# Performance work log

Measured on AMD Instinct MI355X. Metric: run time of the kernel, lower is better.

## Reference

```python
import jax, jax.numpy as jnp
import numpy as np

EDGES = np.array([[0,13],[0,1],[0,4],[0,10],[0,7],[13,14],[14,15],[15,16],[1,2],[2,3],
                  [3,17],[4,5],[5,6],[6,18],[10,11],[11,12],[12,19],[7,8],[8,9],[9,20]])
N = 21
EPS = 1e-5


def _build_adj():
    # adj_mx_from_edges: symmetric binary adjacency + self-loops, row-normalized (D^-1 (A+I))
    A = np.zeros((N, N), np.float32)
    A[EDGES[:, 0], EDGES[:, 1]] = 1.0
    A = np.maximum(A, A.T)
    A = A + np.eye(N, dtype=np.float32)
    A = A / A.sum(1, keepdims=True)
    return A


def setup_inputs() -> dict:
    key = jax.random.key(0)
    ks = jax.random.split(key, 10)
    B, C, H, W = 64, 256, 64, 64
    s = 0.05
    return {
        "feature_s": jax.random.normal(ks[0], (B, C, H, W), jnp.float32),
        "target_s": jax.random.uniform(ks[1], (B, N, H, W), jnp.float32),
        "adj": jnp.asarray(_build_adj()),
        "bn_gamma": jnp.ones((N,), jnp.float32),
        "bn_beta": jnp.zeros((N,), jnp.float32),
        "gru_wx": s * jax.random.normal(ks[2], (256, 768), jnp.float32),
        "gru_wh": s * jax.random.normal(ks[3], (256, 768), jnp.float32),
        "gru_bx": jnp.zeros((768,), jnp.float32),
        "gru_bh": jnp.zeros((768,), jnp.float32),
        "w_g1": s * jax.random.normal(ks[4], (2, 256, 256), jnp.float32),
        "b_g1": jnp.zeros((256,), jnp.float32),
        "w_g2": s * jax.random.normal(ks[5], (2, 256, 256), jnp.float32),
        "b_g2": jnp.zeros((256,), jnp.float32),
        "w_out": s * jax.random.normal(ks[6], (2, 256, 3), jnp.float32),
        "b_out": jnp.zeros((3,), jnp.float32),
    }


def _batchnorm1d(x, gamma, beta):
    # x: [B, 21, C]; BatchNorm1d over channel dim 21 (stats over batch and length)
    mean = jnp.mean(x, axis=(0, 2), keepdims=True)
    var = jnp.var(x, axis=(0, 2), keepdims=True)
    xn = (x - mean) * jax.lax.rsqrt(var + EPS)
    return xn * gamma[None, :, None] + beta[None, :, None]


def _gru(x, wx, wh, bx, bh):
    # standard GRU scanned over the 21-joint axis; x: [B, N, 256] -> [B, N, 256]
    B, n, Hd = x.shape
    xg = jnp.einsum('bnc,ch->bnh', x, wx) + bx  # [B, N, 3H]

    def step(h, xg_t):
        hg = h @ wh + bh
        r = jax.nn.sigmoid(xg_t[..., :Hd] + hg[..., :Hd])
        z = jax.nn.sigmoid(xg_t[..., Hd:2 * Hd] + hg[..., Hd:2 * Hd])
        ncand = jnp.tanh(xg_t[..., 2 * Hd:] + r * hg[..., 2 * Hd:])
        h_new = (1.0 - z) * ncand + z * h
        return h_new, h_new

    h0 = jnp.zeros((B, Hd), x.dtype)
    _, ys = jax.lax.scan(step, h0, jnp.swapaxes(xg, 0, 1))
    return jnp.swapaxes(ys, 0, 1)


def _laplacian(adj):
    # normalized Laplacian L = I - D^{-1/2} A D^{-1/2}
    d = adj.sum(-1)
    dinv = jnp.where(d > 0, jax.lax.rsqrt(jnp.where(d > 0, d, 1.0)), 0.0)
    return jnp.eye(N, dtype=adj.dtype) - dinv[:, None] * adj * dinv[None, :]


def _chebconv(x, L, w, b):
    # K=2 Chebyshev conv: T0 = I, T1 = L ->  x @ W0 + (L x) @ W1 + b
    return jnp.einsum('bnc,co->bno', x, w[0]) + jnp.einsum('nm,bmc,co->bno', L, x, w[1]) + b


def reference(feature_s, target_s, adj, bn_gamma, bn_beta,
              gru_wx, gru_wh, gru_bx, gru_bh,
              w_g1, b_g1, w_g2, b_g2, w_out, b_out):
    B, C, H, W = feature_s.shape
    # batched correlation: [B, 21, HW] x [B, HW, C] -> [B, 21, C]
    q = jnp.einsum('bjp,bcp->bjc',
                   target_s.reshape(B, N, H * W),
                   feature_s.reshape(B, C, H * W))
    q = _batchnorm1d(q, bn_gamma, bn_beta)
    q = jnp.where(q > 0, q, 0.1 * q)  # LeakyReLU(0.1)
    q = _gru(q, gru_wx, gru_wh, gru_bx, gru_bh)
    # _ResChebGC: two graph convs with ReLU + residual (dropout = identity in eval)
    L = _laplacian(adj)
    h = jax.nn.relu(_chebconv(q, L, w_g1, b_g1))
    h = jax.nn.relu(_chebconv(h, L, w_g2, b_g2))
    x = q + h
    return _chebconv(x, L, w_out, b_out)  # [B, 21, 3]
```

## Files before the change

### kernel.cpp

```cpp
#include <hip/hip_runtime.h>
#include <cstdint>

#define B   64
#define NJ  21
#define CHN 256
#define HW  4096
#define G3  768

typedef _Float16 f16x8 __attribute__((ext_vector_type(8)));
typedef float    f32x4 __attribute__((ext_vector_type(4)));
typedef _Float16 f16x2 __attribute__((ext_vector_type(2)));
typedef __fp16   fp16x2v __attribute__((ext_vector_type(2)));
union PKU { fp16x2v h; unsigned u; };
union HU { unsigned u; f16x2 h; };
union FRU { f16x8 v; unsigned u[4]; };

static __device__ inline unsigned pack_f16(float a, float b){
  HU u; u.h.x = (_Float16)a; u.h.y = (_Float16)b; return u.u;
}

static __device__ inline float fdot2f(unsigned wu, unsigned hu, float acc){
  HU w, h; w.u = wu; h.u = hu;
#if __has_builtin(__builtin_amdgcn_fdot2)
  return __builtin_amdgcn_fdot2(w.h, h.h, acc, false);
#else
  return acc + (float)w.h.x*(float)h.h.x + (float)w.h.y*(float)h.h.y;
#endif
}

__global__ __launch_bounds__(64) void k_lap(const float* __restrict__ adj, float* __restrict__ L){
  __shared__ float dinv[NJ];
  int t = threadIdx.x;
  if (t < NJ){
    float s = 0.f;
    for (int j=0;j<NJ;j++) s += adj[t*NJ+j];
    dinv[t] = s > 0.f ? 1.f/sqrtf(s) : 0.f;
  }
  __syncthreads();
  for (int idx=t; idx<NJ*NJ; idx+=64){
    int i = idx/NJ, j = idx%NJ;
    L[idx] = (i==j ? 1.f : 0.f) - dinv[i]*adj[idx]*dinv[j];
  }
}

__global__ __launch_bounds__(512,4) void k_corr6(const float* __restrict__ T,
    const float* __restrict__ F, _Float16* __restrict__ P){
  int bid = blockIdx.x;
  int nb = bid & 1, kb = (bid>>1)&3, b = bid>>3;
  int t = threadIdx.x;
  int w = t>>6, l = t&63;
  __shared__ __align__(16) unsigned short Tl[32*1024];

  for (int i=t; i<5632; i+=512){
    int r = 21 + (i>>9), pr = i & 511;
    int addr = (r*2048 + pr*4) ^ ((r&7)<<4);
    *(unsigned*)((char*)Tl + addr) = 0u;
  }
  {
    const float2* Tp = (const float2*)(T + (size_t)b*NJ*HW + (size_t)kb*1024);
    for (int i=t; i<21*512; i+=512){
      int r = i>>9, pr = i & 511;
      float2 v = Tp[(size_t)r*2048 + pr];
      PKU pk; pk.h = __builtin_amdgcn_cvt_pkrtz(v.x, v.y);
      int addr = (r*2048 + pr*4) ^ ((r&7)<<4);
      *(unsigned*)((char*)Tl + addr) = pk.u;
    }
  }
  __syncthreads();

  int cl = l & 15, kg = l >> 4;
  const float4* Fp = (const float4*)(F + ((size_t)b*CHN + nb*128 + w*16 + cl)*HW
                                       + (size_t)kb*1024) + kg*2;
  f32x4 acc0 = {0.f,0.f,0.f,0.f}, acc1 = {0.f,0.f,0.f,0.f};
  int r = l & 15;
  int swz = (r&7)<<4;

  #pragma unroll 4
  for (int chunk=0; chunk<32; ++chunk){
    float4 f0 = Fp[chunk*8];
    float4 f1 = Fp[chunk*8 + 1];
    FRU bf;
    bf.u[0] = pack_f16(f0.x, f0.y);
    bf.u[1] = pack_f16(f0.z, f0.w);
    bf.u[2] = pack_f16(f1.x, f1.y);
    bf.u[3] = pack_f16(f1.z, f1.w);
    int kbyte = chunk*64 + kg*16;
    f16x8 a0 = *(const f16x8*)((const char*)Tl + ((r*2048      + kbyte) ^ swz));
    f16x8 a1 = *(const f16x8*)((const char*)Tl + (((r+16)*2048 + kbyte) ^ swz));
    acc0 = __builtin_amdgcn_mfma_f32_16x16x32_f16(a0, bf.v, acc0, 0, 0, 0);
    acc1 = __builtin_amdgcn_mfma_f32_16x16x32_f16(a1, bf.v, acc1, 0, 0, 0);
  }

  int cbase = nb*128 + w*16 + (l&15);
  #pragma unroll
  for (int i=0;i<4;i++){
    int row0 = (l>>4)*4 + i;
    if (row0 < 21)
      P[(((size_t)kb*64 + b)*21 + row0)*256 + cbase] = (_Float16)acc0[i];
    int row1 = row0 + 16;
    if (row1 < 21)
      P[(((size_t)kb*64 + b)*21 + row1)*256 + cbase] = (_Float16)acc1[i];
  }
}

__global__ __launch_bounds__(256) void k_stats(const _Float16* __restrict__ P,
    float* __restrict__ q, float* __restrict__ stats){
  int j = blockIdx.x, t = threadIdx.x;
  const size_t KSTRIDE = (size_t)64*21*256;
  float s = 0.f, ss = 0.f;
  for (int b=0;b<B;b++){
    size_t i0 = ((size_t)b*21 + j)*256 + t;
    float v = (float)P[i0] + (float)P[KSTRIDE + i0]
            + (float)P[2*KSTRIDE + i0] + (float)P[3*KSTRIDE + i0];
    q[((size_t)b*NJ + j)*CHN + t] = v;
    s += v; ss += v*v;
  }
  #pragma unroll
  for (int o=32;o>0;o>>=1){ s += __shfl_down(s,o); ss += __shfl_down(ss,o); }
  __shared__ float sb[4], ssb[4];
  int wid = t>>6;
  if ((t&63)==0){ sb[wid]=s; ssb[wid]=ss; }
  __syncthreads();
  if (t==0){
    float S  = sb[0]+sb[1]+sb[2]+sb[3];
    float SS = ssb[0]+ssb[1]+ssb[2]+ssb[3];
    float mean = S * (1.f/16384.f);
    float var  = SS * (1.f/16384.f) - mean*mean;
    stats[j]      = mean;
    stats[NJ + j] = 1.f/sqrtf(var + 1e-5f);
  }
}

__global__ __launch_bounds__(256) void k_xg(const float* __restrict__ q,
    const float* __restrict__ stats, const float* __restrict__ gamma, const float* __restrict__ beta,
    const float* __restrict__ wx, const float* __restrict__ bx, float* __restrict__ xg){
  int b = blockIdx.x/3, sl = blockIdx.x%3;
  int t = threadIdx.x;
  int col = sl*256 + t;
  __shared__ float xn[NJ][CHN];
  for (int idx=t; idx<NJ*CHN; idx+=256){
    int j = idx >> 8;
    float v = (q[(size_t)b*NJ*CHN + idx] - stats[j]) * stats[NJ+j];
    v = v * gamma[j] + beta[j];
    xn[j][idx & 255] = v > 0.f ? v : 0.1f*v;
  }
  __syncthreads();
  float acc[NJ];
  #pragma unroll
  for (int j=0;j<NJ;j++) acc[j]=0.f;
  for (int c=0;c<CHN;c++){
    float wv = wx[(size_t)c*G3 + col];
    #pragma unroll
    for (int j=0;j<NJ;j++) acc[j] += xn[j][c]*wv;
  }
  float bv = bx[col];
  #pragma unroll
  for (int j=0;j<NJ;j++) xg[((size_t)b*NJ+j)*G3 + col] = acc[j] + bv;
}

__global__ __launch_bounds__(256) void k_pack(const float* __restrict__ wh, unsigned* __restrict__ whp){
  int idx = blockIdx.x*256 + threadIdx.x;
  int c2 = idx / G3, col = idx % G3;
  float w0 = wh[(size_t)(2*c2)*G3 + col];
  float w1 = wh[(size_t)(2*c2+1)*G3 + col];
  whp[idx] = pack_f16(w0, w1);
}

__global__ __launch_bounds__(768,3) void k_gru(const unsigned* __restrict__ whp,
    const float* __restrict__ bh, const float* __restrict__ xg, float* __restrict__ gout){
  int b = blockIdx.x;
  int col = threadIdx.x;
  int l = col & 63;
  __shared__ float hf[256];
  __shared__ float lr[256], lz[256];
  unsigned wr[64];
  #pragma unroll
  for (int i=0;i<64;i++) wr[i] = whp[i*G3 + col];
  const unsigned* wsp = whp + 64*G3 + col;
  float bhv = bh[col];
  if (col < 256) hf[col] = 0.f;
  unsigned hv0 = 0u, hv1 = 0u;
  float xv_next = xg[((size_t)b*NJ + 0)*G3 + col];
  __syncthreads();
  for (int step=0; step<NJ; ++step){
    float xvc = xv_next;
    if (step < NJ-1) xv_next = xg[((size_t)b*NJ + step+1)*G3 + col];
    float a0 = 0.f, a1 = 0.f;
    #pragma unroll
    for (int i=0;i<64;i++)
      a1 = fdot2f(wsp[(size_t)i*G3], __builtin_amdgcn_readlane(hv1, i), a1);
    #pragma unroll
    for (int i=0;i<64;i++)
      a0 = fdot2f(wr[i], __builtin_amdgcn_readlane(hv0, i), a0);
    float a = a0 + a1 + bhv;
    if (col < 256)      lr[col]     = 1.f/(1.f+__expf(-(xvc + a)));
    else if (col < 512) lz[col-256] = 1.f/(1.f+__expf(-(xvc + a)));
    __syncthreads();
    if (col >= 512){
      int i = col - 512;
      float nv = tanhf(xvc + lr[i]*a);
      float z  = lz[i];
      float hnew = (1.f - z)*nv + z*hf[i];
      gout[((size_t)b*NJ + step)*CHN + i] = hnew;
      hf[i] = hnew;
    }
    __syncthreads();
    float2 p0 = *(const float2*)&hf[2*l];
    float2 p1 = *(const float2*)&hf[128 + 2*l];
    hv0 = pack_f16(p0.x, p0.y);
    hv1 = pack_f16(p1.x, p1.y);
  }
}

__global__ __launch_bounds__(256) void k_cheb(const float* __restrict__ xin,
    const float* __restrict__ Lm, const float* __restrict__ W,
    const float* __restrict__ bvec, float* __restrict__ out){
  int b = blockIdx.x >> 2, oq = blockIdx.x & 3;
  int t = threadIdx.x;
  int ol = t & 63, ck = t >> 6;
  __shared__ float xs[NJ][CHN];
  __shared__ float lx[NJ][CHN];
  __shared__ float part[4][64][NJ];
  for (int idx=t; idx<NJ*CHN; idx+=256) xs[idx>>8][idx&255] = xin[(size_t)b*NJ*CHN + idx];
  __syncthreads();
  for (int idx=t; idx<NJ*CHN; idx+=256){
    int j = idx>>8, c = idx&255;
    float sacc = 0.f;
    #pragma unroll
    for (int m=0;m<NJ;m++) sacc += Lm[j*NJ+m]*xs[m][c];
    lx[j][c] = sacc;
  }
  __syncthreads();
  int o = oq*64 + ol;
  float acc[NJ];
  #pragma unroll
  for (int j=0;j<NJ;j++) acc[j]=0.f;
  const float* W0 = W;
  const float* W1 = W + CHN*CHN;
  for (int cc=0; cc<64; ++cc){
    int c = ck*64 + cc;
    float w0 = W0[(size_t)c*CHN + o];
    float w1 = W1[(size_t)c*CHN + o];
    #pragma unroll
    for (int j=0;j<NJ;j++){ acc[j] += xs[j][c]*w0; acc[j] += lx[j][c]*w1; }
  }
  #pragma unroll
  for (int j=0;j<NJ;j++) part[ck][ol][j] = acc[j];
  __syncthreads();
  for (int idx=t; idx<64*NJ; idx+=256){
    int o2 = idx & 63, j = idx >> 6;
    float s2 = part[0][o2][j]+part[1][o2][j]+part[2][o2][j]+part[3][o2][j] + bvec[oq*64+o2];
    s2 = s2 > 0.f ? s2 : 0.f;
    out[(size_t)b*NJ*CHN + j*CHN + oq*64 + o2] = s2;
  }
}

__global__ __launch_bounds__(64) void k_out(const float* __restrict__ gq, const float* __restrict__ h2,
    const float* __restrict__ Lm, const float* __restrict__ W, const float* __restrict__ bvec,
    float* __restrict__ out){
  int b = blockIdx.x, t = threadIdx.x;
  __shared__ float xs[NJ][CHN];
  __shared__ float lx[NJ][CHN];
  for (int idx=t; idx<NJ*CHN; idx+=64)
    xs[idx>>8][idx&255] = gq[(size_t)b*NJ*CHN+idx] + h2[(size_t)b*NJ*CHN+idx];
  __syncthreads();
  for (int idx=t; idx<NJ*CHN; idx+=64){
    int j = idx>>8, c = idx&255;
    float s = 0.f;
    #pragma unroll
    for (int m=0;m<NJ;m++) s += Lm[j*NJ+m]*xs[m][c];
    lx[j][c] = s;
  }
  __syncthreads();
  if (t < 63){
    int j = t/3, o = t%3;
    float acc = bvec[o];
    const float* W0 = W;
    const float* W1 = W + CHN*3;
    for (int c=0;c<CHN;c++){
      acc += xs[j][c]*W0[c*3+o];
      acc += lx[j][c]*W1[c*3+o];
    }
    out[(size_t)b*63 + t] = acc;
  }
}

extern "C" void kernel_launch(void* const* d_in, const int* in_sizes, int n_in,
                              void* d_out, int out_size, void* d_ws, size_t ws_size,
                              hipStream_t stream){
  const float* feat  = (const float*)d_in[0];
  const float* targ  = (const float*)d_in[1];
  const float* adj   = (const float*)d_in[2];
  const float* gamma = (const float*)d_in[3];
  const float* beta  = (const float*)d_in[4];
  const float* wx    = (const float*)d_in[5];
  const float* wh    = (const float*)d_in[6];
  const float* bx    = (const float*)d_in[7];
  const float* bh    = (const float*)d_in[8];
  const float* wg1   = (const float*)d_in[9];
  const float* bg1   = (const float*)d_in[10];
  const float* wg2   = (const float*)d_in[11];
  const float* bg2   = (const float*)d_in[12];
  const float* wout  = (const float*)d_in[13];
  const float* bout  = (const float*)d_in[14];

  float* ws   = (float*)d_ws;
  float* q     = ws + 0;
  float* stats = ws + 400000;
  float* Lw    = ws + 400128;
  float* xgw   = ws + 500000;
  float* gout  = ws + 1600000;
  float* h1    = ws + 2000000;
  float* h2b   = ws + 2400000;
  unsigned* whp = (unsigned*)(ws + 2800000);
  _Float16* P  = (_Float16*)(ws + 3000000);

  k_lap  <<<1,    64, 0, stream>>>(adj, Lw);
  k_pack <<<384, 256, 0, stream>>>(wh, whp);
  k_corr6<<<512, 512, 0, stream>>>(targ, feat, P);
  k_stats<<<21,  256, 0, stream>>>(P, q, stats);
  k_xg   <<<192, 256, 0, stream>>>(q, stats, gamma, beta, wx, bx, xgw);
  k_gru  <<<64,  768, 0, stream>>>(whp, bh, xgw, gout);
  k_cheb <<<256, 256, 0, stream>>>(gout, Lw, wg1, bg1, h1);
  k_cheb <<<256, 256, 0, stream>>>(h1,   Lw, wg2, bg2, h2b);
  k_out  <<<64,   64, 0, stream>>>(gout, h2b, Lw, wout, bout, (float*)d_out);
}
```

Before: 262.3 us.

## Stream feature tiles via async global-to-LDS loads with triple buffering in correlation kernel

The correlation kernel now splits HW into 8 K-chunks instead of 4, doubling the grid to 1024 blocks and halving each block's T tile in LDS. Feature loads go directly to LDS through global_load_lds into a 3-slot ring buffer per wave, with explicit vmcnt waits so loads stay in flight while the MFMAs run. The stats kernel now sums 8 partial products instead of 4. This trades more LDS use and twice as much partial-sum traffic for better memory-level parallelism on the bandwidth-bound feature stream.

```diff
diff --git a/kernel.cpp b/kernel.cpp
--- a/kernel.cpp
+++ b/kernel.cpp
@@ -28,6 +28,17 @@
 #endif
 }
 
+static __device__ __forceinline__ void gload_lds16(const float* g, float* l){
+#if __has_builtin(__builtin_amdgcn_global_load_lds)
+  __builtin_amdgcn_global_load_lds((const __attribute__((address_space(1))) void*)g,
+                                   (__attribute__((address_space(3))) void*)l, 16, 0, 0);
+#else
+  int lane = threadIdx.x & 63;
+  f32x4 v = *(const f32x4*)g;
+  *(f32x4*)((char*)l + lane*16) = v;
+#endif
+}
+
 __global__ __launch_bounds__(64) void k_lap(const float* __restrict__ adj, float* __restrict__ L){
   __shared__ float dinv[NJ];
   int t = threadIdx.x;
@@ -43,52 +54,66 @@
   }
 }
 
-__global__ __launch_bounds__(512,4) void k_corr6(const float* __restrict__ T,
+__global__ __launch_bounds__(512,4) void k_corr7(const float* __restrict__ T,
     const float* __restrict__ F, _Float16* __restrict__ P){
   int bid = blockIdx.x;
-  int nb = bid & 1, kb = (bid>>1)&3, b = bid>>3;
+  int nb = bid & 1, kb = (bid>>1)&7, b = bid>>4;
   int t = threadIdx.x;
   int w = t>>6, l = t&63;
-  __shared__ __align__(16) unsigned short Tl[32*1024];
-
-  for (int i=t; i<5632; i+=512){
-    int r = 21 + (i>>9), pr = i & 511;
-    int addr = (r*2048 + pr*4) ^ ((r&7)<<4);
-    *(unsigned*)((char*)Tl + addr) = 0u;
+  __shared__ __align__(16) unsigned short Tl[32*512];
+  __shared__ __align__(16) float Fl[8][3][512];
+
+  for (int i=t; i<2816; i+=512){
+    int r = 21 + i/256, wo = i%256;
+    *(unsigned*)((char*)Tl + (r*1024 + ((wo*4) ^ ((r&7)<<4)))) = 0u;
   }
   {
-    const float2* Tp = (const float2*)(T + (size_t)b*NJ*HW + (size_t)kb*1024);
-    for (int i=t; i<21*512; i+=512){
-      int r = i>>9, pr = i & 511;
+    const float2* Tp = (const float2*)(T + (size_t)b*NJ*HW + (size_t)kb*512);
+    for (int i=t; i<21*256; i+=512){
+      int r = i>>8, pr = i&255;
       float2 v = Tp[(size_t)r*2048 + pr];
       PKU pk; pk.h = __builtin_amdgcn_cvt_pkrtz(v.x, v.y);
-      int addr = (r*2048 + pr*4) ^ ((r&7)<<4);
-      *(unsigned*)((char*)Tl + addr) = pk.u;
+      *(unsigned*)((char*)Tl + (r*1024 + ((pr*4) ^ ((r&7)<<4)))) = pk.u;
     }
   }
   __syncthreads();
 
   int cl = l & 15, kg = l >> 4;
-  const float4* Fp = (const float4*)(F + ((size_t)b*CHN + nb*128 + w*16 + cl)*HW
-                                       + (size_t)kb*1024) + kg*2;
+  const float* gsrc = F + ((size_t)b*CHN + nb*128 + w*16 + cl)*HW + (size_t)kb*512 + kg*8;
+  float* slotbase = &Fl[w][0][0];
+
   f32x4 acc0 = {0.f,0.f,0.f,0.f}, acc1 = {0.f,0.f,0.f,0.f};
-  int r = l & 15;
+  int r = cl;
   int swz = (r&7)<<4;
-
-  #pragma unroll 4
-  for (int chunk=0; chunk<32; ++chunk){
-    float4 f0 = Fp[chunk*8];
-    float4 f1 = Fp[chunk*8 + 1];
+  const char* TlB = (const char*)Tl;
+
+  gload_lds16(gsrc + 0*32,     slotbase);
+  gload_lds16(gsrc + 0*32 + 4, slotbase + 256);
+  gload_lds16(gsrc + 1*32,     slotbase + 512);
+  gload_lds16(gsrc + 1*32 + 4, slotbase + 512 + 256);
+
+  #pragma unroll
+  for (int c=0; c<16; ++c){
+    int cc = (c+2 < 16) ? (c+2) : 15;
+    float* lpn = slotbase + ((c+2)%3)*512;
+    gload_lds16(gsrc + cc*32,     lpn);
+    gload_lds16(gsrc + cc*32 + 4, lpn + 256);
+    asm volatile("s_waitcnt vmcnt(4)" ::: "memory");
+    __builtin_amdgcn_sched_barrier(0);
+    const char* sp = (const char*)(slotbase + (c%3)*512);
+    f32x4 v0 = *(const f32x4*)(sp + l*16);
+    f32x4 v1 = *(const f32x4*)(sp + 1024 + l*16);
     FRU bf;
-    bf.u[0] = pack_f16(f0.x, f0.y);
-    bf.u[1] = pack_f16(f0.z, f0.w);
-    bf.u[2] = pack_f16(f1.x, f1.y);
-    bf.u[3] = pack_f16(f1.z, f1.w);
-    int kbyte = chunk*64 + kg*16;
-    f16x8 a0 = *(const f16x8*)((const char*)Tl + ((r*2048      + kbyte) ^ swz));
-    f16x8 a1 = *(const f16x8*)((const char*)Tl + (((r+16)*2048 + kbyte) ^ swz));
+    bf.u[0] = pack_f16(v0[0], v0[1]);
+    bf.u[1] = pack_f16(v0[2], v0[3]);
+    bf.u[2] = pack_f16(v1[0], v1[1]);
+    bf.u[3] = pack_f16(v1[2], v1[3]);
+    int kbyte = c*64 + kg*16;
+    f16x8 a0 = *(const f16x8*)(TlB + (r*1024      + (kbyte ^ swz)));
+    f16x8 a1 = *(const f16x8*)(TlB + ((r+16)*1024 + (kbyte ^ swz)));
     acc0 = __builtin_amdgcn_mfma_f32_16x16x32_f16(a0, bf.v, acc0, 0, 0, 0);
     acc1 = __builtin_amdgcn_mfma_f32_16x16x32_f16(a1, bf.v, acc1, 0, 0, 0);
+    __builtin_amdgcn_sched_barrier(0);
   }
 
   int cbase = nb*128 + w*16 + (l&15);
@@ -110,8 +135,9 @@
   float s = 0.f, ss = 0.f;
   for (int b=0;b<B;b++){
     size_t i0 = ((size_t)b*21 + j)*256 + t;
-    float v = (float)P[i0] + (float)P[KSTRIDE + i0]
-            + (float)P[2*KSTRIDE + i0] + (float)P[3*KSTRIDE + i0];
+    float v = 0.f;
+    #pragma unroll
+    for (int k=0;k<8;k++) v += (float)P[k*KSTRIDE + i0];
     q[((size_t)b*NJ + j)*CHN + t] = v;
     s += v; ss += v*v;
   }
@@ -317,7 +343,7 @@
 
   k_lap  <<<1,    64, 0, stream>>>(adj, Lw);
   k_pack <<<384, 256, 0, stream>>>(wh, whp);
-  k_corr6<<<512, 512, 0, stream>>>(targ, feat, P);
+  k_corr7<<<1024,512, 0, stream>>>(targ, feat, P);
   k_stats<<<21,  256, 0, stream>>>(P, q, stats);
   k_xg   <<<192, 256, 0, stream>>>(q, stats, gamma, beta, wx, bx, xgw);
   k_gru  <<<64,  768, 0, stream>>>(whp, bh, xgw, gout);
```

Result: slower. 275.3 us (+5.0%).
